# Optimization experiments

Measured on AMD Instinct MI355X. Metric: run time of the kernel, lower is better.

## Reference

```python
import jax, jax.numpy as jnp
import numpy as np

N, D, H, K, C = 8192, 1024, 512, 16, 9  # patches, embed, hidden, heads, classes


def setup_inputs() -> dict:
    key = jax.random.key(0)
    ks = jax.random.split(key, 20)
    sD = 1.0 / np.sqrt(D)
    sH = 1.0 / np.sqrt(H)
    inp = {
        "x": jax.random.normal(ks[0], (N, D), jnp.float32),
        # gated attention heads, stacked over K heads; weights stored [in, out]
        "Vw": jax.random.normal(ks[1], (K, D, H), jnp.float32) * sD,
        "Vb": jax.random.normal(ks[2], (K, H), jnp.float32) * sD,
        "Uw": jax.random.normal(ks[3], (K, D, H), jnp.float32) * sD,
        "Ub": jax.random.normal(ks[4], (K, H), jnp.float32) * sD,
        "ww": jax.random.normal(ks[5], (K, H), jnp.float32) * sH,
        "wb": jax.random.normal(ks[6], (K,), jnp.float32) * sH,
        # average-pooling head MLP: D -> H -> D
        "pW1": jax.random.normal(ks[7], (D, H), jnp.float32) * sD,
        "pb1": jax.random.normal(ks[8], (H,), jnp.float32) * sD,
        "pW2": jax.random.normal(ks[9], (H, D), jnp.float32) * sH,
        "pb2": jax.random.normal(ks[10], (D,), jnp.float32) * sH,
        # classifier: D -> 1024 -> 512 -> 256 -> C
        "cW1": jax.random.normal(ks[11], (D, 1024), jnp.float32) * sD,
        "cb1": jax.random.normal(ks[12], (1024,), jnp.float32) * sD,
        "cW2": jax.random.normal(ks[13], (1024, 512), jnp.float32) * (1.0 / np.sqrt(1024)),
        "cb2": jax.random.normal(ks[14], (512,), jnp.float32) * (1.0 / np.sqrt(1024)),
        "cW3": jax.random.normal(ks[15], (512, 256), jnp.float32) * (1.0 / np.sqrt(512)),
        "cb3": jax.random.normal(ks[16], (256,), jnp.float32) * (1.0 / np.sqrt(512)),
        "cW4": jax.random.normal(ks[17], (256, C), jnp.float32) * (1.0 / np.sqrt(256)),
        "cb4": jax.random.normal(ks[18], (C,), jnp.float32) * (1.0 / np.sqrt(256)),
    }
    return inp


def reference(x, Vw, Vb, Uw, Ub, ww, wb, pW1, pb1, pW2, pb2,
              cW1, cb1, cW2, cb2, cW3, cb3, cW4, cb4):
    # --- multi-head gated attention (all K heads batched) ---
    AV = jnp.tanh(jnp.einsum('nd,kdh->knh', x, Vw) + Vb[:, None, :])          # [K,N,H]
    AU = jax.nn.sigmoid(jnp.einsum('nd,kdh->knh', x, Uw) + Ub[:, None, :])    # [K,N,H]
    scores = jnp.einsum('knh,kh->kn', AV * AU, ww) + wb[:, None]              # [K,N]
    A = jax.nn.softmax(scores, axis=1)                                        # softmax over patches
    agg_heads = jnp.einsum('kn,nd->kd', A, x)                                 # [K,D]
    # --- average pooling head: mean over patches then MLP D->H->D ---
    m = jnp.mean(x, axis=0)
    avg_agg = jax.nn.relu(m @ pW1 + pb1) @ pW2 + pb2                          # [D]
    # --- mean over all K+1 heads ---
    aggregated = (jnp.sum(agg_heads, axis=0) + avg_agg) / (K + 1)             # [D]
    # --- classifier (eval mode: dropout = identity) ---
    h = jax.nn.relu(aggregated @ cW1 + cb1)
    h = jax.nn.relu(h @ cW2 + cb2)
    h = jax.nn.relu(h @ cW3 + cb3)
    logits = h @ cW4 + cb4                                                    # [C]
    # eval mode applies softmax (not self.training branch)
    return jax.nn.softmax(logits, axis=-1)
```

## Files before the change

### kernel.cpp

```cpp
#include <hip/hip_runtime.h>
#include <stdint.h>

#define N_PATCH 8192
#define DIM     1024
#define HID     512
#define NHEAD   16

using i32x4 = __attribute__((ext_vector_type(4))) int;

__device__ __forceinline__ void gload_lds16(const void* g, void* l) {
  __builtin_amdgcn_global_load_lds(
      reinterpret_cast<const __attribute__((address_space(1))) void*>(
          reinterpret_cast<uintptr_t>(g)),
      reinterpret_cast<__attribute__((address_space(3))) void*>(
          reinterpret_cast<uintptr_t>(l)),
      16, 0, 0);
}

__device__ __forceinline__ int q8(float v, float rs) {
  int q = (int)rintf(v * rs);
  return q > 127 ? 127 : (q < -127 ? -127 : q);
}

__global__ void prep1_kernel(const float* __restrict__ x,
                             signed char* __restrict__ xq, float* __restrict__ sx,
                             const float* __restrict__ Vw, const float* __restrict__ Uw,
                             float* __restrict__ swp, float* __restrict__ rswp) {
  __shared__ __align__(16) float red4[16][16][4];
  const int bid = blockIdx.x;
  const int t = threadIdx.x;
  if (bid < 2048) {
    const int row = bid * 4 + (t >> 6);
    const int lane = t & 63;
    const float* xr = x + (size_t)row * DIM;
    float4 v[4];
    float am = 0.f;
    #pragma unroll
    for (int j = 0; j < 4; ++j) {
      v[j] = *(const float4*)&xr[j * 256 + lane * 4];
      am = fmaxf(am, fmaxf(fmaxf(fabsf(v[j].x), fabsf(v[j].y)),
                           fmaxf(fabsf(v[j].z), fabsf(v[j].w))));
    }
    #pragma unroll
    for (int s = 32; s; s >>= 1) am = fmaxf(am, __shfl_xor(am, s, 64));
    const float rs = (am > 0.f) ? 127.f / am : 0.f;
    #pragma unroll
    for (int j = 0; j < 4; ++j) {
      int b = (q8(v[j].x, rs) & 255) | ((q8(v[j].y, rs) & 255) << 8) |
              ((q8(v[j].z, rs) & 255) << 16) | ((q8(v[j].w, rs) & 255) << 24);
      ((int*)xq)[row * 256 + j * 64 + lane] = b;
    }
    if (lane == 0) sx[row] = am / 127.f;
    return;
  }
  const int b2 = bid - 2048;
  const int u = b2 >> 7, k = (b2 >> 3) & 15, hc = b2 & 7;
  const float* W = u ? Uw : Vw;
  const int h4 = t & 15, dseg = t >> 4;
  const size_t base = (size_t)k * DIM * HID + hc * 64 + h4 * 4;
  float4 am4 = {0.f, 0.f, 0.f, 0.f};
  for (int i = 0; i < 64; ++i) {
    float4 v = *(const float4*)&W[base + (size_t)(dseg * 64 + i) * HID];
    am4.x = fmaxf(am4.x, fabsf(v.x));
    am4.y = fmaxf(am4.y, fabsf(v.y));
    am4.z = fmaxf(am4.z, fabsf(v.z));
    am4.w = fmaxf(am4.w, fabsf(v.w));
  }
  *(float4*)&red4[dseg][h4][0] = am4;
  __syncthreads();
  if (t < 64) {
    float m = 0.f;
    #pragma unroll
    for (int ds = 0; ds < 16; ++ds) m = fmaxf(m, red4[ds][t >> 2][t & 3]);
    const int h = hc * 64 + t;
    const int c = (h >> 4) * 32 + u * 16 + (h & 15);
    swp[k * 1024 + c]  = m / 127.f;
    rswp[k * 1024 + c] = (m > 0.f) ? 127.f / m : 0.f;
  }
}

__global__ void pack_wq_kernel(const float* __restrict__ Vw,
                               const float* __restrict__ Uw,
                               const float* __restrict__ rswp,
                               signed char* __restrict__ Wq) {
  __shared__ __align__(16) signed char T[128][80];
  const int bid = blockIdx.x;
  const int k = bid >> 7, hc = (bid >> 4) & 7, dc = bid & 15;
  const int t = threadIdx.x;
  const int d0 = dc * 64, h0 = hc * 64;
  const int hh = t & 63;
  const size_t base = (size_t)k * DIM * HID;
  #pragma unroll
  for (int u = 0; u < 2; ++u) {
    const float* W = u ? Uw : Vw;
    const int h = h0 + hh;
    const int cl = ((hh >> 4) << 5) + (u << 4) + (hh & 15);
    const float rs = rswp[k * 1024 + hc * 128 + cl];
    #pragma unroll
    for (int i = 0; i < 16; ++i) {
      const int dd = i * 4 + (t >> 6);
      T[cl][dd] = (signed char)q8(W[base + (size_t)(d0 + dd) * HID + h], rs);
    }
  }
  __syncthreads();
  #pragma unroll
  for (int j = 0; j < 2; ++j) {
    const int idx = j * 256 + t;
    const int cl = idx >> 2, dq = idx & 3;
    i32x4 val = *(const i32x4*)&T[cl][dq * 16];
    const size_t col = (size_t)k * 1024 + hc * 128 + cl;
    *(i32x4*)&Wq[col * DIM + d0 + dq * 16] = val;
  }
}

__global__ __launch_bounds__(512, 1) void gemm_scores_kernel(
    const signed char* __restrict__ xq, const signed char* __restrict__ Wq,
    const float* __restrict__ sx, const float* __restrict__ swp,
    const float* __restrict__ Vb, const float* __restrict__ Ub,
    const float* __restrict__ ww, float* __restrict__ part) {
  __shared__ __align__(16) signed char As[2][16384];
  __shared__ __align__(16) signed char Bs[2][16384];
  const int bid = blockIdx.x;
  const int x8 = bid & 7;
  const int s  = (bid >> 3) & 31;
  const int w  = bid >> 8;
  const int mt = (x8 & 1) * 16 + (w & 1) * 8 + (s >> 2);
  const int ct = (x8 >> 1) * 16 + (w >> 1) * 4 + (s & 3);
  const int kh = ct >> 2, cb = ct & 3;
  const int tid = threadIdx.x;
  const int wv = tid >> 6, lane = tid & 63;
  const int wr = wv >> 2, wc = wv & 3;
  const int l15 = lane & 15, l4 = lane >> 4;

  const signed char* Ab = xq + (size_t)mt * 256 * DIM;
  const signed char* Bb = Wq + (size_t)ct * 256 * DIM;

  i32x4 acc[8][4];
  #pragma unroll
  for (int i = 0; i < 8; ++i)
    #pragma unroll
    for (int j = 0; j < 4; ++j) acc[i][j] = (i32x4){0, 0, 0, 0};

  auto stageA = [&](int t) {
    const int buf = t & 1, db = t << 6;
    #pragma unroll
    for (int p = 0; p < 2; ++p) {
      const int r = p * 128 + (tid >> 2);
      const int ksrc = ((tid & 3) * 16) ^ (((r >> 1) & 3) << 4);
      gload_lds16(Ab + (size_t)r * DIM + db + ksrc,
                  (char*)&As[buf][0] + p * 8192 + wv * 1024);
    }
  };
  auto stageB = [&](int t) {
    const int buf = t & 1, db = t << 6;
    #pragma unroll
    for (int p = 0; p < 2; ++p) {
      const int r = p * 128 + (tid >> 2);
      const int ksrc = ((tid & 3) * 16) ^ (((r >> 1) & 3) << 4);
      gload_lds16(Bb + (size_t)r * DIM + db + ksrc,
                  (char*)&Bs[buf][0] + p * 8192 + wv * 1024);
    }
  };

  const int swz = ((l15 >> 1) & 3) << 4;
  const int kb0 = (l4 * 16) ^ swz;
  const int aB0 = wr * 8192 + l15 * 64 + kb0;
  const int bB0 = wc * 4096 + l15 * 64 + kb0;

  i32x4 a[8], b[4];

  stageA(0); stageB(0); stageA(1); stageB(1);
  __syncthreads();

  for (int u = 0; u < 16; ++u) {
    const int buf = u & 1;
    const char* Abase = (const char*)&As[buf][0];
    const char* Bbase = (const char*)&Bs[buf][0];
    #pragma unroll
    for (int f = 0; f < 8; ++f) a[f] = *(const i32x4*)(Abase + aB0 + f * 1024);
    #pragma unroll
    for (int nf = 0; nf < 4; ++nf) b[nf] = *(const i32x4*)(Bbase + bB0 + nf * 1024);
    if (u < 15) { stageA(u + 1); stageB(u + 1); }
    __builtin_amdgcn_s_setprio(1);
    #pragma unroll
    for (int f = 0; f < 8; ++f)
      #pragma unroll
      for (int nf = 0; nf < 4; ++nf)
        acc[f][nf] = __builtin_amdgcn_mfma_i32_16x16x64_i8(a[f], b[nf], acc[f][nf], 0, 0, 0);
    __builtin_amdgcn_s_setprio(0);
    __syncthreads();
  }

  float partial[8][4];
  #pragma unroll
  for (int f = 0; f < 8; ++f)
    #pragma unroll
    for (int r = 0; r < 4; ++r) partial[f][r] = 0.f;

  float vb[2], ub[2], wwv[2], swv[2], swu[2];
  #pragma unroll
  for (int p = 0; p < 2; ++p) {
    const int hl = (cb * 8 + wc * 2 + p) * 16 + l15;
    vb[p]  = Vb[kh * HID + hl];
    ub[p]  = Ub[kh * HID + hl];
    wwv[p] = ww[kh * HID + hl];
    swv[p] = swp[ct * 256 + wc * 64 + (2 * p) * 16 + l15];
    swu[p] = swp[ct * 256 + wc * 64 + (2 * p + 1) * 16 + l15];
  }
  const int rbase = mt * 256 + wr * 128 + l4 * 4;
  #pragma unroll
  for (int f = 0; f < 8; ++f) {
    const float4 sx4 = *(const float4*)&sx[rbase + f * 16];
    const float sxr[4] = {sx4.x, sx4.y, sx4.z, sx4.w};
    #pragma unroll
    for (int p = 0; p < 2; ++p)
      #pragma unroll
      for (int r = 0; r < 4; ++r) {
        const float scv = (float)acc[f][2 * p][r] * (sxr[r] * swv[p]) + vb[p];
        const float scu = (float)acc[f][2 * p + 1][r] * (sxr[r] * swu[p]) + ub[p];
        const float e2 = __expf(2.f * scv);
        const float av = 1.f - 2.f / (e2 + 1.f);
        const float au = 1.f / (1.f + __expf(-scu));
        partial[f][r] += av * au * wwv[p];
      }
  }
  #pragma unroll
  for (int s2 = 1; s2 < 16; s2 <<= 1)
    #pragma unroll
    for (int f = 0; f < 8; ++f)
      #pragma unroll
      for (int r = 0; r < 4; ++r)
        partial[f][r] += __shfl_xor(partial[f][r], s2, 64);

  if (l15 == 0) {
    const int j = cb * 4 + wc;
    float* dst = part + ((size_t)j * NHEAD + kh) * N_PATCH;
    #pragma unroll
    for (int f = 0; f < 8; ++f)
      #pragma unroll
      for (int r = 0; r < 4; ++r)
        dst[rbase + f * 16 + r] = partial[f][r];
  }
}

__global__ void scores_part_kernel(const float* __restrict__ part,
                                   float* __restrict__ scores,
                                   float* __restrict__ spart) {
  const int k = blockIdx.x >> 3, c = blockIdx.x & 7;
  const int t = threadIdx.x;
  __shared__ float shm[4], shs[4];
  float v[4];
  float mx = -1e30f;
  #pragma unroll
  for (int i = 0; i < 4; ++i) {
    const int n = c * 1024 + i * 256 + t;
    float s = 0.f;
    #pragma unroll
    for (int j = 0; j < 16; ++j) s += part[((size_t)j * NHEAD + k) * N_PATCH + n];
    v[i] = s;
    scores[(size_t)k * N_PATCH + n] = s;
    mx = fmaxf(mx, s);
  }
  #pragma unroll
  for (int sft = 32; sft; sft >>= 1) mx = fmaxf(mx, __shfl_xor(mx, sft, 64));
  const int wv = t >> 6;
  if ((t & 63) == 0) shm[wv] = mx;
  __syncthreads();
  mx = fmaxf(fmaxf(shm[0], shm[1]), fmaxf(shm[2], shm[3]));
  float sum = 0.f;
  #pragma unroll
  for (int i = 0; i < 4; ++i) sum += __expf(v[i] - mx);
  #pragma unroll
  for (int sft = 32; sft; sft >>= 1) sum += __shfl_xor(sum, sft, 64);
  if ((t & 63) == 0) shs[wv] = sum;
  __syncthreads();
  if (t == 0) {
    spart[(k * 8 + c) * 2]     = mx;
    spart[(k * 8 + c) * 2 + 1] = shs[0] + shs[1] + shs[2] + shs[3];
  }
}

__global__ void weighted_part_kernel(const signed char* __restrict__ xq,
                                     const float* __restrict__ sx,
                                     const float* __restrict__ scores,
                                     const float* __restrict__ spart,
                                     float* __restrict__ wp1,
                                     float* __restrict__ wp2) {
  __shared__ float wsx[128], s2x[128];
  __shared__ float sm[16], srz[16];
  const int d = blockIdx.x * 256 + threadIdx.x;
  const int nc = blockIdx.y;
  if (threadIdx.x < 16) {
    const int k = threadIdx.x;
    float m = -1e30f;
    #pragma unroll
    for (int c = 0; c < 8; ++c) m = fmaxf(m, spart[(k * 8 + c) * 2]);
    float S = 0.f;
    #pragma unroll
    for (int c = 0; c < 8; ++c)
      S += spart[(k * 8 + c) * 2 + 1] * __expf(spart[(k * 8 + c) * 2] - m);
    sm[k] = m; srz[k] = 1.f / S;
  }
  __syncthreads();
  if (threadIdx.x < 128) {
    const int n = nc * 128 + threadIdx.x;
    float s = 0.f;
    #pragma unroll
    for (int k = 0; k < NHEAD; ++k)
      s += __expf(scores[(size_t)k * N_PATCH + n] - sm[k]) * srz[k];
    const float sxn = sx[n];
    wsx[threadIdx.x] = s * sxn;
    s2x[threadIdx.x] = sxn;
  }
  __syncthreads();
  float a1 = 0.f, a2 = 0.f;
  for (int i = 0; i < 128; ++i) {
    const float q = (float)xq[(size_t)(nc * 128 + i) * DIM + d];
    a1 += wsx[i] * q;
    a2 += s2x[i] * q;
  }
  wp1[nc * DIM + d] = a1;
  wp2[nc * DIM + d] = a2;
}

__global__ void reduce_vec_kernel(const float* __restrict__ wp1,
                                  const float* __restrict__ wp2,
                                  float* __restrict__ y1,
                                  float* __restrict__ mvec) {
  int d = blockIdx.x * 256 + threadIdx.x;
  float s1 = 0.f, s2 = 0.f;
  #pragma unroll
  for (int i = 0; i < 64; ++i) {
    s1 += wp1[i * DIM + d];
    s2 += wp2[i * DIM + d];
  }
  y1[d] = s1;
  mvec[d] = s2 * (1.f / (float)N_PATCH);
}

__global__ void gemv_fused_kernel(const float* __restrict__ in,
                                  const float* __restrict__ W,
                                  const float* __restrict__ bias,
                                  const float* __restrict__ extra, float scale,
                                  int do_relu, float* __restrict__ out,
                                  int In, int Out) {
  __shared__ float red[4][64];
  const int jl = threadIdx.x & 63, kc = threadIdx.x >> 6;
  const int j = blockIdx.x * 64 + jl;
  const int chunk = In >> 2;
  const float* Wp = W + (size_t)(kc * chunk) * Out + j;
  const float* ip = in + kc * chunk;
  float acc = 0.f;
  #pragma unroll 4
  for (int d = 0; d < chunk; ++d) acc += ip[d] * Wp[(size_t)d * Out];
  if (kc) red[kc][jl] = acc;
  __syncthreads();
  if (kc == 0) {
    float v = bias[j] + acc + red[1][jl] + red[2][jl] + red[3][jl];
    if (extra) v += extra[j];
    v *= scale;
    if (do_relu) v = fmaxf(v, 0.f);
    out[j] = v;
  }
}

__global__ void c3_final_kernel(const float* __restrict__ c2,
                                const float* __restrict__ W3,
                                const float* __restrict__ b3,
                                const float* __restrict__ W4,
                                const float* __restrict__ b4,
                                float* __restrict__ out) {
  __shared__ float c3s[256];
  __shared__ float logits[9];
  const int t = threadIdx.x;
  float acc = b3[t];
  #pragma unroll 4
  for (int d = 0; d < 512; ++d) acc += c2[d] * W3[(size_t)d * 256 + t];
  c3s[t] = fmaxf(acc, 0.f);
  __syncthreads();
  if (t < 9) {
    float l = b4[t];
    for (int d = 0; d < 256; ++d) l += c3s[d] * W4[d * 9 + t];
    logits[t] = l;
  }
  __syncthreads();
  if (t == 0) {
    float mx = logits[0];
    for (int j = 1; j < 9; ++j) mx = fmaxf(mx, logits[j]);
    float e[9], s = 0.f;
    for (int j = 0; j < 9; ++j) { e[j] = expf(logits[j] - mx); s += e[j]; }
    for (int j = 0; j < 9; ++j) out[j] = e[j] / s;
  }
}

extern "C" void kernel_launch(void* const* d_in, const int* in_sizes, int n_in,
                              void* d_out, int out_size, void* d_ws, size_t ws_size,
                              hipStream_t stream) {
  (void)in_sizes; (void)n_in; (void)out_size; (void)ws_size;
  const float* x   = (const float*)d_in[0];
  const float* Vw  = (const float*)d_in[1];
  const float* Vb  = (const float*)d_in[2];
  const float* Uw  = (const float*)d_in[3];
  const float* Ub  = (const float*)d_in[4];
  const float* ww  = (const float*)d_in[5];
  const float* pW1 = (const float*)d_in[7];
  const float* pb1 = (const float*)d_in[8];
  const float* pW2 = (const float*)d_in[9];
  const float* pb2 = (const float*)d_in[10];
  const float* cW1 = (const float*)d_in[11];
  const float* cb1 = (const float*)d_in[12];
  const float* cW2 = (const float*)d_in[13];
  const float* cb2 = (const float*)d_in[14];
  const float* cW3 = (const float*)d_in[15];
  const float* cb3 = (const float*)d_in[16];
  const float* cW4 = (const float*)d_in[17];
  const float* cb4 = (const float*)d_in[18];
  float* out = (float*)d_out;

  char* ws = (char*)d_ws;
  size_t o = 0;
  auto alloc = [&](size_t bytes) -> char* {
    char* p = ws + o;
    o += (bytes + 255) & ~(size_t)255;
    return p;
  };
  signed char* xq = (signed char*)alloc((size_t)N_PATCH * DIM);
  signed char* Wq = (signed char*)alloc((size_t)NHEAD * 1024 * DIM);
  float* sx    = (float*)alloc(N_PATCH * 4);
  float* swp   = (float*)alloc(NHEAD * 1024 * 4);
  float* rswp  = (float*)alloc(NHEAD * 1024 * 4);
  float* part  = (float*)alloc((size_t)16 * NHEAD * N_PATCH * 4);
  float* scores= (float*)alloc((size_t)NHEAD * N_PATCH * 4);
  float* spart = (float*)alloc(NHEAD * 8 * 2 * 4);
  float* wp1   = (float*)alloc(64 * DIM * 4);
  float* wp2   = (float*)alloc(64 * DIM * 4);
  float* y1    = (float*)alloc(DIM * 4);
  float* mvec  = (float*)alloc(DIM * 4);
  float* h1    = (float*)alloc(HID * 4);
  float* aggr  = (float*)alloc(DIM * 4);
  float* c1    = (float*)alloc(1024 * 4);
  float* c2    = (float*)alloc(512 * 4);

  prep1_kernel<<<2304, 256, 0, stream>>>(x, xq, sx, Vw, Uw, swp, rswp);
  pack_wq_kernel<<<2048, 256, 0, stream>>>(Vw, Uw, rswp, Wq);
  gemm_scores_kernel<<<2048, 512, 0, stream>>>(xq, Wq, sx, swp, Vb, Ub, ww, part);
  scores_part_kernel<<<128, 256, 0, stream>>>(part, scores, spart);
  weighted_part_kernel<<<dim3(4, 64), 256, 0, stream>>>(xq, sx, scores, spart, wp1, wp2);
  reduce_vec_kernel<<<4, 256, 0, stream>>>(wp1, wp2, y1, mvec);
  gemv_fused_kernel<<<8, 256, 0, stream>>>(mvec, pW1, pb1, nullptr, 1.f, 1, h1, DIM, HID);
  gemv_fused_kernel<<<16, 256, 0, stream>>>(h1, pW2, pb2, y1, 1.f / 17.f, 0, aggr, HID, DIM);
  gemv_fused_kernel<<<16, 256, 0, stream>>>(aggr, cW1, cb1, nullptr, 1.f, 1, c1, 1024, 1024);
  gemv_fused_kernel<<<8, 256, 0, stream>>>(c1, cW2, cb2, nullptr, 1.f, 1, c2, 1024, 512);
  c3_final_kernel<<<1, 256, 0, stream>>>(c2, cW3, cb3, cW4, cb4, out);
}
```

Before: 388.1 us.

## Double K-tile depth in int8 scores GEMM and split staging into halves

The int8 MFMA scores GEMM now stages 128-wide K slices instead of 64, so the main loop runs 8 iterations instead of 16 and performs half as many block barriers. Each slice is loaded in two halves interleaved with two rounds of MFMAs, using a second register set for the second K half and a wider 8-way XOR swizzle in LDS. Shared memory use grows to 128 KB per block and register pressure rises with the extra fragments, which risks spills or lower occupancy.

Result: no change. 384.2 us (-1.0%).

```diff
diff --git a/kernel.cpp b/kernel.cpp
--- a/kernel.cpp
+++ b/kernel.cpp
@@ -118,8 +118,8 @@
     const float* __restrict__ sx, const float* __restrict__ swp,
     const float* __restrict__ Vb, const float* __restrict__ Ub,
     const float* __restrict__ ww, float* __restrict__ part) {
-  __shared__ __align__(16) signed char As[2][16384];
-  __shared__ __align__(16) signed char Bs[2][16384];
+  __shared__ __align__(16) signed char As[2][32768];
+  __shared__ __align__(16) signed char Bs[2][32768];
   const int bid = blockIdx.x;
   const int x8 = bid & 7;
   const int s  = (bid >> 3) & 31;
@@ -141,52 +141,68 @@
     #pragma unroll
     for (int j = 0; j < 4; ++j) acc[i][j] = (i32x4){0, 0, 0, 0};
 
-  auto stageA = [&](int t) {
-    const int buf = t & 1, db = t << 6;
-    #pragma unroll
-    for (int p = 0; p < 2; ++p) {
-      const int r = p * 128 + (tid >> 2);
-      const int ksrc = ((tid & 3) * 16) ^ (((r >> 1) & 3) << 4);
+  auto stageA_h = [&](int t, int half) {
+    const int buf = t & 1, db = t << 7;
+    #pragma unroll
+    for (int pp = 0; pp < 2; ++pp) {
+      const int p = half * 2 + pp;
+      const int r = p * 64 + (tid >> 3);
+      const int ksrc = ((tid & 7) * 16) ^ (((r >> 1) & 7) << 4);
       gload_lds16(Ab + (size_t)r * DIM + db + ksrc,
                   (char*)&As[buf][0] + p * 8192 + wv * 1024);
     }
   };
-  auto stageB = [&](int t) {
-    const int buf = t & 1, db = t << 6;
-    #pragma unroll
-    for (int p = 0; p < 2; ++p) {
-      const int r = p * 128 + (tid >> 2);
-      const int ksrc = ((tid & 3) * 16) ^ (((r >> 1) & 3) << 4);
+  auto stageB_h = [&](int t, int half) {
+    const int buf = t & 1, db = t << 7;
+    #pragma unroll
+    for (int pp = 0; pp < 2; ++pp) {
+      const int p = half * 2 + pp;
+      const int r = p * 64 + (tid >> 3);
+      const int ksrc = ((tid & 7) * 16) ^ (((r >> 1) & 7) << 4);
       gload_lds16(Bb + (size_t)r * DIM + db + ksrc,
                   (char*)&Bs[buf][0] + p * 8192 + wv * 1024);
     }
   };
 
-  const int swz = ((l15 >> 1) & 3) << 4;
-  const int kb0 = (l4 * 16) ^ swz;
-  const int aB0 = wr * 8192 + l15 * 64 + kb0;
-  const int bB0 = wc * 4096 + l15 * 64 + kb0;
-
-  i32x4 a[8], b[4];
-
-  stageA(0); stageB(0); stageA(1); stageB(1);
-  __syncthreads();
-
-  for (int u = 0; u < 16; ++u) {
+  const int swz = ((l15 >> 1) & 7) << 4;
+  const int kb0 = (0 * 64 + l4 * 16) ^ swz;
+  const int kb1 = (1 * 64 + l4 * 16) ^ swz;
+  const int aRow = (wr * 128 + l15) * 128;
+  const int bRow = (wc * 64 + l15) * 128;
+
+  i32x4 a[8], b[4], a2[8], b2[4];
+
+  stageA_h(0, 0); stageA_h(0, 1); stageB_h(0, 0); stageB_h(0, 1);
+  stageA_h(1, 0); stageA_h(1, 1); stageB_h(1, 0); stageB_h(1, 1);
+  __syncthreads();
+
+  for (int u = 0; u < 8; ++u) {
     const int buf = u & 1;
     const char* Abase = (const char*)&As[buf][0];
     const char* Bbase = (const char*)&Bs[buf][0];
     #pragma unroll
-    for (int f = 0; f < 8; ++f) a[f] = *(const i32x4*)(Abase + aB0 + f * 1024);
-    #pragma unroll
-    for (int nf = 0; nf < 4; ++nf) b[nf] = *(const i32x4*)(Bbase + bB0 + nf * 1024);
-    if (u < 15) { stageA(u + 1); stageB(u + 1); }
+    for (int f = 0; f < 8; ++f) a[f] = *(const i32x4*)(Abase + aRow + f * 2048 + kb0);
+    #pragma unroll
+    for (int nf = 0; nf < 4; ++nf) b[nf] = *(const i32x4*)(Bbase + bRow + nf * 2048 + kb0);
+    if (u < 7) { stageA_h(u + 1, 0); stageB_h(u + 1, 0); }
+    #pragma unroll
+    for (int f = 0; f < 8; ++f) a2[f] = *(const i32x4*)(Abase + aRow + f * 2048 + kb1);
+    #pragma unroll
+    for (int nf = 0; nf < 4; ++nf) b2[nf] = *(const i32x4*)(Bbase + bRow + nf * 2048 + kb1);
     __builtin_amdgcn_s_setprio(1);
     #pragma unroll
     for (int f = 0; f < 8; ++f)
       #pragma unroll
       for (int nf = 0; nf < 4; ++nf)
         acc[f][nf] = __builtin_amdgcn_mfma_i32_16x16x64_i8(a[f], b[nf], acc[f][nf], 0, 0, 0);
+    __builtin_amdgcn_s_setprio(0);
+    if (u < 7) { stageA_h(u + 1, 1); stageB_h(u + 1, 1); }
+    __builtin_amdgcn_s_setprio(1);
+    #pragma unroll
+    for (int f = 0; f < 8; ++f)
+      #pragma unroll
+      for (int nf = 0; nf < 4; ++nf)
+        acc[f][nf] = __builtin_amdgcn_mfma_i32_16x16x64_i8(a2[f], b2[nf], acc[f][nf], 0, 0, 0);
     __builtin_amdgcn_s_setprio(0);
     __syncthreads();
   }
```
